# Performance work log

Hardware: AMD Instinct MI355X
Metric: run time of the kernel (lower is better)

## Reference

```python
import jax, jax.numpy as jnp
import numpy as np

N = 50000      # nodes
E = 800000     # edges (before self loops)
IN, HID, OUT = 128, 64, 64
H = 2          # heads (concat=False -> mean over heads)
NEG_SLOPE = 0.2


def setup_inputs() -> dict:
    key = jax.random.key(0)
    ks = jax.random.split(key, 10)
    s = 0.1
    x = jax.random.normal(ks[0], (N, IN), jnp.float32)
    edge_index = jax.random.randint(ks[1], (2, E), 0, N, dtype=jnp.int64)
    W1 = jax.random.normal(ks[2], (IN, H * HID), jnp.float32) * s
    att_src1 = jax.random.normal(ks[3], (H, HID), jnp.float32) * s
    att_dst1 = jax.random.normal(ks[4], (H, HID), jnp.float32) * s
    bias1 = jnp.zeros((HID,), jnp.float32)
    W2 = jax.random.normal(ks[5], (HID, H * OUT), jnp.float32) * s
    att_src2 = jax.random.normal(ks[6], (H, OUT), jnp.float32) * s
    att_dst2 = jax.random.normal(ks[7], (H, OUT), jnp.float32) * s
    bias2 = jnp.zeros((OUT,), jnp.float32)
    return dict(x=x, edge_index=edge_index, W1=W1, att_src1=att_src1,
                att_dst1=att_dst1, bias1=bias1, W2=W2, att_src2=att_src2,
                att_dst2=att_dst2, bias2=bias2)


def gat_conv(x, src, dst, W, a_src, a_dst, bias, heads, ch):
    n = x.shape[0]
    h = (x @ W).reshape(n, heads, ch)                 # [N,H,C]
    e_src = jnp.sum(h * a_src, axis=-1)               # [N,H]
    e_dst = jnp.sum(h * a_dst, axis=-1)               # [N,H]
    e = jax.nn.leaky_relu(e_src[src] + e_dst[dst], NEG_SLOPE)  # [E',H]
    # segment softmax over edges grouped by destination node
    m = jax.ops.segment_max(e, dst, num_segments=n)
    m = jnp.where(jnp.isfinite(m), m, 0.0)
    ex = jnp.exp(e - m[dst])
    denom = jax.ops.segment_sum(ex, dst, num_segments=n) + 1e-16
    alpha = ex / denom[dst]                            # [E',H]
    out = jax.ops.segment_sum(alpha[:, :, None] * h[src], dst, num_segments=n)
    return out.mean(axis=1) + bias                     # [N,C]


def reference(x, edge_index, W1, att_src1, att_dst1, bias1,
              W2, att_src2, att_dst2, bias2):
    loop = jnp.arange(N, dtype=edge_index.dtype)
    src = jnp.concatenate([edge_index[0], loop])       # add self loops
    dst = jnp.concatenate([edge_index[1], loop])
    h = gat_conv(x, src, dst, W1, att_src1, att_dst1, bias1, H, HID)
    h = jax.nn.relu(h)
    out = gat_conv(h, src, dst, W2, att_src2, att_dst2, bias2, H, OUT)
    return out
```

## Files before the change

### kernel.cpp

```cpp
#include <hip/hip_runtime.h>
#include <hip/hip_fp16.h>
#include <math.h>


#define IN_DIM 128
#define FLATC 128

__device__ __forceinline__ float lrelu02(float t) {
    return t > 0.f ? t : 0.2f * t;
}


__global__ void count_kernel(const int* __restrict__ dst, int* __restrict__ cnt, int e) {
    int i = blockIdx.x * blockDim.x + threadIdx.x;
    if (i < e) atomicAdd(&cnt[dst[i]], 1);
}

__global__ __launch_bounds__(256) void scan_bsum(const int* __restrict__ cnt,
                                                 int* __restrict__ bsum, int n) {
    __shared__ int red[256];
    int t = threadIdx.x;
    int i = blockIdx.x * 256 + t;
    red[t] = (i < n) ? cnt[i] + 1 : 0;
    __syncthreads();
#pragma unroll
    for (int off = 128; off > 0; off >>= 1) {
        if (t < off) red[t] += red[t + off];
        __syncthreads();
    }
    if (t == 0) bsum[blockIdx.x] = red[0];
}

__global__ __launch_bounds__(1024) void scan_boff(const int* __restrict__ bsum,
                                                  int* __restrict__ boff,
                                                  int* __restrict__ row_start,
                                                  int nb, int n) {
    __shared__ int s[1024];
    int t = threadIdx.x;
    int v = (t < nb) ? bsum[t] : 0;
    s[t] = v;
    __syncthreads();
    for (int off = 1; off < 1024; off <<= 1) {
        int u = (t >= off) ? s[t - off] : 0;
        __syncthreads();
        s[t] += u;
        __syncthreads();
    }
    if (t < nb) boff[t] = s[t] - v;
    if (t == nb - 1) row_start[n] = s[t];
}

__global__ __launch_bounds__(256) void scan_write(const int* __restrict__ cnt,
                                                  const int* __restrict__ boff,
                                                  int* __restrict__ row_start,
                                                  int* __restrict__ cursor,
                                                  int* __restrict__ adj, int n) {
    __shared__ int s[256];
    int t = threadIdx.x;
    int i = blockIdx.x * 256 + t;
    int v = (i < n) ? cnt[i] + 1 : 0;
    s[t] = v;
    __syncthreads();
    for (int off = 1; off < 256; off <<= 1) {
        int u = (t >= off) ? s[t - off] : 0;
        __syncthreads();
        s[t] += u;
        __syncthreads();
    }
    if (i < n) {
        int rs = boff[blockIdx.x] + s[t] - v;
        row_start[i] = rs;
        adj[rs] = i;
        cursor[i] = rs + 1;
    }
}

__global__ void scatter_kernel(const int* __restrict__ src, const int* __restrict__ dst,
                               int* __restrict__ cursor, int* __restrict__ adj, int e) {
    int i = blockIdx.x * blockDim.x + threadIdx.x;
    if (i < e) {
        int d = dst[i];
        int pos = atomicAdd(&cursor[d], 1);
        adj[pos] = src[i];
    }
}


__global__ __launch_bounds__(256) void gemm64_dots(const float* __restrict__ A,
                                                   const float* __restrict__ B,
                                                   __half* __restrict__ h16,
                                                   const float* __restrict__ att_s,
                                                   const float* __restrict__ att_d,
                                                   float2* __restrict__ es2,
                                                   float2* __restrict__ ed2,
                                                   int nrows, int K) {
    __shared__ float As[64][33];
    __shared__ float Bs[32][128];
    const int tid = threadIdx.x;
    const int tx = tid & 15;
    const int ty = tid >> 4;
    const int row0 = blockIdx.x * 64;

    float acc[4][8];
#pragma unroll
    for (int r = 0; r < 4; ++r)
#pragma unroll
        for (int c = 0; c < 8; ++c) acc[r][c] = 0.f;

    for (int k0 = 0; k0 < K; k0 += 32) {
#pragma unroll
        for (int i = 0; i < 2; ++i) {
            int idx = tid + i * 256;
            int r = idx >> 3;
            int c4 = (idx & 7) * 4;
            float4 v = make_float4(0.f, 0.f, 0.f, 0.f);
            int row = row0 + r;
            if (row < nrows) v = *(const float4*)(A + (size_t)row * K + k0 + c4);
            As[r][c4 + 0] = v.x; As[r][c4 + 1] = v.y;
            As[r][c4 + 2] = v.z; As[r][c4 + 3] = v.w;
        }
#pragma unroll
        for (int i = 0; i < 4; ++i) {
            int idx = tid + i * 256;
            int r = idx >> 5;
            int c4 = (idx & 31) * 4;
            float4 v = *(const float4*)(B + (size_t)(k0 + r) * FLATC + c4);
            *(float4*)&Bs[r][c4] = v;
        }
        __syncthreads();
#pragma unroll
        for (int kk = 0; kk < 32; ++kk) {
            float a[4], b[8];
#pragma unroll
            for (int r = 0; r < 4; ++r) a[r] = As[ty * 4 + r][kk];
#pragma unroll
            for (int c = 0; c < 8; ++c) b[c] = Bs[kk][tx + 16 * c];
#pragma unroll
            for (int r = 0; r < 4; ++r)
#pragma unroll
                for (int c = 0; c < 8; ++c) acc[r][c] = fmaf(a[r], b[c], acc[r][c]);
        }
        __syncthreads();
    }

    float asr[8], adr[8];
#pragma unroll
    for (int c = 0; c < 8; ++c) {
        asr[c] = att_s[tx + 16 * c];
        adr[c] = att_d[tx + 16 * c];
    }
#pragma unroll
    for (int r = 0; r < 4; ++r) {
        int row = row0 + ty * 4 + r;
        float s0 = 0.f, s1 = 0.f, d0 = 0.f, d1 = 0.f;
#pragma unroll
        for (int c = 0; c < 4; ++c) {
            s0 = fmaf(acc[r][c], asr[c], s0);
            d0 = fmaf(acc[r][c], adr[c], d0);
        }
#pragma unroll
        for (int c = 4; c < 8; ++c) {
            s1 = fmaf(acc[r][c], asr[c], s1);
            d1 = fmaf(acc[r][c], adr[c], d1);
        }
#pragma unroll
        for (int m = 1; m < 16; m <<= 1) {
            s0 += __shfl_xor(s0, m);
            s1 += __shfl_xor(s1, m);
            d0 += __shfl_xor(d0, m);
            d1 += __shfl_xor(d1, m);
        }
        if (row < nrows) {
#pragma unroll
            for (int c = 0; c < 8; ++c)
                h16[(size_t)row * FLATC + tx + 16 * c] = __float2half_rn(acc[r][c]);
            if (tx == 0) {
                es2[row] = make_float2(s0, s1);
                ed2[row] = make_float2(d0, d1);
            }
        }
    }
}


__global__ __launch_bounds__(256) void softmax_alpha(const int* __restrict__ row_start,
                                                     const int* __restrict__ adj,
                                                     const float2* __restrict__ es2,
                                                     const float2* __restrict__ ed2,
                                                     float2* __restrict__ alpha2,
                                                     int n) {
    int node = blockIdx.x * 4 + (threadIdx.x >> 6);
    if (node >= n) return;
    const int lane = threadIdx.x & 63;
    const int beg = row_start[node];
    const int end = row_start[node + 1];
    const float2 edv = ed2[node];

    if (end - beg <= 64) {
        int j = beg + lane;
        bool act = j < end;
        int id = adj[act ? j : beg];
        float2 ev = es2[id];
        float f0 = lrelu02(ev.x + edv.x);
        float f1 = lrelu02(ev.y + edv.y);
        float m0 = act ? f0 : -3.0e38f;
        float m1 = act ? f1 : -3.0e38f;
#pragma unroll
        for (int off = 1; off < 64; off <<= 1) {
            m0 = fmaxf(m0, __shfl_xor(m0, off));
            m1 = fmaxf(m1, __shfl_xor(m1, off));
        }
        float p0 = act ? expf(f0 - m0) : 0.f;
        float p1 = act ? expf(f1 - m1) : 0.f;
        float s0 = p0, s1 = p1;
#pragma unroll
        for (int off = 1; off < 64; off <<= 1) {
            s0 += __shfl_xor(s0, off);
            s1 += __shfl_xor(s1, off);
        }
        if (act)
            alpha2[j] = make_float2(p0 / (s0 + 1e-16f), p1 / (s1 + 1e-16f));
        return;
    }

    float m0 = -3.0e38f, m1 = -3.0e38f;
    float s0 = 0.f, s1 = 0.f;
    for (int j = beg + lane; j < end; j += 64) {
        float2 ev = es2[adj[j]];
        float f0 = lrelu02(ev.x + edv.x);
        float f1 = lrelu02(ev.y + edv.y);
        float mn0 = fmaxf(m0, f0);
        s0 = s0 * expf(m0 - mn0) + expf(f0 - mn0);
        m0 = mn0;
        float mn1 = fmaxf(m1, f1);
        s1 = s1 * expf(m1 - mn1) + expf(f1 - mn1);
        m1 = mn1;
    }
#pragma unroll
    for (int off = 1; off < 64; off <<= 1) {
        float mo0 = __shfl_xor(m0, off), so0 = __shfl_xor(s0, off);
        float mo1 = __shfl_xor(m1, off), so1 = __shfl_xor(s1, off);
        float mn0 = fmaxf(m0, mo0);
        s0 = s0 * expf(m0 - mn0) + so0 * expf(mo0 - mn0);
        m0 = mn0;
        float mn1 = fmaxf(m1, mo1);
        s1 = s1 * expf(m1 - mn1) + so1 * expf(mo1 - mn1);
        m1 = mn1;
    }
    const float inv0 = 1.f / (s0 + 1e-16f);
    const float inv1 = 1.f / (s1 + 1e-16f);
    for (int j = beg + lane; j < end; j += 64) {
        float2 ev = es2[adj[j]];
        float f0 = lrelu02(ev.x + edv.x);
        float f1 = lrelu02(ev.y + edv.y);
        alpha2[j] = make_float2(expf(f0 - m0) * inv0, expf(f1 - m1) * inv1);
    }
}


__global__ __launch_bounds__(256) void agg(const int* __restrict__ row_start,
                                           const int* __restrict__ adj,
                                           const __half2* __restrict__ h16,
                                           const float2* __restrict__ alpha2,
                                           const float* __restrict__ bias,
                                           float* __restrict__ out,
                                           int n, int do_relu) {
    int node = blockIdx.x * 4 + (threadIdx.x >> 6);
    if (node >= n) return;
    const int lane = threadIdx.x & 63;
    const int head = lane >> 5;
    const int beg = row_start[node];
    const int end = row_start[node + 1];
    const __half2* hp = h16 + lane;

    float ax = 0.f, ay = 0.f;
    int j = beg;
    for (; j + 4 <= end; j += 4) {
        int i0 = adj[j], i1 = adj[j + 1], i2 = adj[j + 2], i3 = adj[j + 3];
        float2 a0 = alpha2[j], a1 = alpha2[j + 1];
        float2 a2 = alpha2[j + 2], a3 = alpha2[j + 3];
        __half2 v0 = hp[(size_t)i0 * 64];
        __half2 v1 = hp[(size_t)i1 * 64];
        __half2 v2 = hp[(size_t)i2 * 64];
        __half2 v3 = hp[(size_t)i3 * 64];
        float w0 = head ? a0.y : a0.x;
        float w1 = head ? a1.y : a1.x;
        float w2 = head ? a2.y : a2.x;
        float w3 = head ? a3.y : a3.x;
        float2 f0 = __half22float2(v0);
        float2 f1 = __half22float2(v1);
        float2 f2 = __half22float2(v2);
        float2 f3 = __half22float2(v3);
        ax = fmaf(w0, f0.x, ax); ay = fmaf(w0, f0.y, ay);
        ax = fmaf(w1, f1.x, ax); ay = fmaf(w1, f1.y, ay);
        ax = fmaf(w2, f2.x, ax); ay = fmaf(w2, f2.y, ay);
        ax = fmaf(w3, f3.x, ax); ay = fmaf(w3, f3.y, ay);
    }
    for (; j < end; ++j) {
        int i0 = adj[j];
        float2 a0 = alpha2[j];
        float w0 = head ? a0.y : a0.x;
        float2 f0 = __half22float2(hp[(size_t)i0 * 64]);
        ax = fmaf(w0, f0.x, ax); ay = fmaf(w0, f0.y, ay);
    }

    float ox = 0.5f * (ax + __shfl_xor(ax, 32));
    float oy = 0.5f * (ay + __shfl_xor(ay, 32));
    if (lane < 32) {
        int c = 2 * lane;
        ox += bias[c];
        oy += bias[c + 1];
        if (do_relu) { ox = fmaxf(ox, 0.f); oy = fmaxf(oy, 0.f); }
        *(float2*)(out + (size_t)node * 64 + c) = make_float2(ox, oy);
    }
}


extern "C" void kernel_launch(void* const* d_in, const int* in_sizes, int n_in,
                              void* d_out, int out_size, void* d_ws, size_t ws_size,
                              hipStream_t stream) {
    const float* x   = (const float*)d_in[0];
    const int*   ei  = (const int*)d_in[1];
    const float* W1  = (const float*)d_in[2];
    const float* as1 = (const float*)d_in[3];
    const float* ad1 = (const float*)d_in[4];
    const float* b1  = (const float*)d_in[5];
    const float* W2  = (const float*)d_in[6];
    const float* as2 = (const float*)d_in[7];
    const float* ad2 = (const float*)d_in[8];
    const float* b2  = (const float*)d_in[9];

    const int N_ = in_sizes[0] / IN_DIM;
    const int E_ = in_sizes[1] / 2;
    const int* src = ei;
    const int* dst = ei + E_;
    const int TOT = E_ + N_;

    auto align16 = [](size_t v) { return (v + 15) & ~(size_t)15; };
    char* p = (char*)d_ws;
    int* cnt       = (int*)p; p += align16((size_t)N_ * 4);
    int* row_start = (int*)p; p += align16((size_t)(N_ + 1) * 4);
    int* cursor    = (int*)p; p += align16((size_t)N_ * 4);
    int* adj       = (int*)p; p += align16((size_t)TOT * 4);
    int* bsum      = (int*)p; p += align16((size_t)1024 * 4);
    int* boff      = (int*)p; p += align16((size_t)1024 * 4);
    __half* h16    = (__half*)p; p += align16((size_t)N_ * FLATC * 2);
    float* out1    = (float*)p; p += align16((size_t)N_ * 64 * 4);
    float* es      = (float*)p; p += align16((size_t)N_ * 2 * 4);
    float* ed      = (float*)p; p += align16((size_t)N_ * 2 * 4);
    float* alpha   = (float*)p; p += align16((size_t)TOT * 2 * 4);
    (void)ws_size; (void)n_in; (void)out_size;

    const int NB = (N_ + 255) / 256;

    hipMemsetAsync(cnt, 0, (size_t)N_ * 4, stream);
    count_kernel<<<(E_ + 255) / 256, 256, 0, stream>>>(dst, cnt, E_);
    scan_bsum<<<NB, 256, 0, stream>>>(cnt, bsum, N_);
    scan_boff<<<1, 1024, 0, stream>>>(bsum, boff, row_start, NB, N_);
    scan_write<<<NB, 256, 0, stream>>>(cnt, boff, row_start, cursor, adj, N_);
    scatter_kernel<<<(E_ + 255) / 256, 256, 0, stream>>>(src, dst, cursor, adj, E_);

    const int gG = (N_ + 63) / 64;
    const int gN4 = (N_ + 3) / 4;

    gemm64_dots<<<gG, 256, 0, stream>>>(x, W1, h16, as1, ad1,
                                        (float2*)es, (float2*)ed, N_, IN_DIM);
    softmax_alpha<<<gN4, 256, 0, stream>>>(row_start, adj, (const float2*)es,
                                           (const float2*)ed, (float2*)alpha, N_);
    agg<<<gN4, 256, 0, stream>>>(row_start, adj, (const __half2*)h16,
                                 (const float2*)alpha, b1, out1, N_, 1);

    gemm64_dots<<<gG, 256, 0, stream>>>(out1, W2, h16, as2, ad2,
                                        (float2*)es, (float2*)ed, N_, 64);
    softmax_alpha<<<gN4, 256, 0, stream>>>(row_start, adj, (const float2*)es,
                                           (const float2*)ed, (float2*)alpha, N_);
    agg<<<gN4, 256, 0, stream>>>(row_start, adj, (const __half2*)h16,
                                 (const float2*)alpha, b2, (float*)d_out, N_, 0);
}
```

Before: 368.3 us.

## Bucket edge scatter by destination range and vectorize GEMM shared-memory reads

The CSR build now records each edge's rank from the counting atomic. Edges are first partitioned into destination buckets of 512 nodes through per-block shared histograms, then a per-bucket kernel writes adj entries, so global writes become localized instead of randomly scattered atomics. The GEMM stores the A tile transposed and reads A and B as float4, assigning contiguous column groups per thread so fp16 outputs are written as half2. This adds an extra rank buffer, an 8-byte pair staging buffer and two more launches, and the bucket histogram assumes no more than 128 buckets.

```diff
diff --git a/kernel.cpp b/kernel.cpp
--- a/kernel.cpp
+++ b/kernel.cpp
@@ -5,15 +5,17 @@
 
 #define IN_DIM 128
 #define FLATC 128
+#define BKT_SHIFT 9
 
 __device__ __forceinline__ float lrelu02(float t) {
     return t > 0.f ? t : 0.2f * t;
 }
 
 
-__global__ void count_kernel(const int* __restrict__ dst, int* __restrict__ cnt, int e) {
+__global__ void count_kernel(const int* __restrict__ dst, int* __restrict__ cnt,
+                             int* __restrict__ rank, int e) {
     int i = blockIdx.x * blockDim.x + threadIdx.x;
-    if (i < e) atomicAdd(&cnt[dst[i]], 1);
+    if (i < e) rank[i] = atomicAdd(&cnt[dst[i]], 1);
 }
 
 __global__ __launch_bounds__(256) void scan_bsum(const int* __restrict__ cnt,
@@ -53,7 +55,6 @@
 __global__ __launch_bounds__(256) void scan_write(const int* __restrict__ cnt,
                                                   const int* __restrict__ boff,
                                                   int* __restrict__ row_start,
-                                                  int* __restrict__ cursor,
                                                   int* __restrict__ adj, int n) {
     __shared__ int s[256];
     int t = threadIdx.x;
@@ -71,17 +72,74 @@
         int rs = boff[blockIdx.x] + s[t] - v;
         row_start[i] = rs;
         adj[rs] = i;
-        cursor[i] = rs + 1;
-    }
-}
-
-__global__ void scatter_kernel(const int* __restrict__ src, const int* __restrict__ dst,
-                               int* __restrict__ cursor, int* __restrict__ adj, int e) {
-    int i = blockIdx.x * blockDim.x + threadIdx.x;
-    if (i < e) {
-        int d = dst[i];
-        int pos = atomicAdd(&cursor[d], 1);
-        adj[pos] = src[i];
+    }
+}
+
+__global__ void init_gcur(const int* __restrict__ row_start, int* __restrict__ gcur,
+                          int nbk, int n) {
+    int b = blockIdx.x * 256 + threadIdx.x;
+    if (b < nbk) {
+        int node = b << BKT_SHIFT;
+        gcur[b] = row_start[node < n ? node : n];
+    }
+}
+
+__global__ __launch_bounds__(256) void bucket_pairs(const int* __restrict__ src,
+                                                    const int* __restrict__ dst,
+                                                    const int* __restrict__ rank,
+                                                    const int* __restrict__ row_start,
+                                                    int* __restrict__ gcur,
+                                                    int2* __restrict__ bstore,
+                                                    int e, int nbk) {
+    __shared__ int hist[128], lbase[128], lcur[128];
+    const int tid = threadIdx.x;
+    const int base = blockIdx.x * 4096;
+    for (int b = tid; b < nbk; b += 256) hist[b] = 0;
+    __syncthreads();
+
+    int myb[16], mypos[16], mys[16];
+#pragma unroll
+    for (int k = 0; k < 16; ++k) {
+        int e0 = base + k * 256 + tid;
+        if (e0 < e) {
+            int d = dst[e0];
+            int b = d >> BKT_SHIFT;
+            myb[k] = b;
+            mypos[k] = row_start[d] + 1 + rank[e0];
+            mys[k] = src[e0];
+            atomicAdd(&hist[b], 1);
+        } else {
+            myb[k] = -1;
+        }
+    }
+    __syncthreads();
+    for (int b = tid; b < nbk; b += 256) {
+        int h = hist[b];
+        lbase[b] = h ? atomicAdd(&gcur[b], h) : 0;
+        lcur[b] = 0;
+    }
+    __syncthreads();
+#pragma unroll
+    for (int k = 0; k < 16; ++k) {
+        if (myb[k] >= 0) {
+            int off = atomicAdd(&lcur[myb[k]], 1);
+            bstore[lbase[myb[k]] + off] = make_int2(mypos[k], mys[k]);
+        }
+    }
+}
+
+__global__ __launch_bounds__(256) void scatter_local(const int* __restrict__ row_start,
+                                                     const int* __restrict__ gcur,
+                                                     const int2* __restrict__ bstore,
+                                                     int* __restrict__ adj,
+                                                     int n) {
+    int b = blockIdx.x;
+    int node = b << BKT_SHIFT;
+    int lo = row_start[node < n ? node : n];
+    int hi = gcur[b];
+    for (int i = lo + threadIdx.x; i < hi; i += 256) {
+        int2 p = bstore[i];
+        adj[p.x] = p.y;
     }
 }
 
@@ -94,18 +152,18 @@
                                                    float2* __restrict__ es2,
                                                    float2* __restrict__ ed2,
                                                    int nrows, int K) {
-    __shared__ float As[64][33];
+    __shared__ float Ast[32][68];
     __shared__ float Bs[32][128];
     const int tid = threadIdx.x;
     const int tx = tid & 15;
     const int ty = tid >> 4;
     const int row0 = blockIdx.x * 64;
 
-    float acc[4][8];
+    float acc0[4][4], acc1[4][4];
 #pragma unroll
     for (int r = 0; r < 4; ++r)
 #pragma unroll
-        for (int c = 0; c < 8; ++c) acc[r][c] = 0.f;
+        for (int c = 0; c < 4; ++c) { acc0[r][c] = 0.f; acc1[r][c] = 0.f; }
 
     for (int k0 = 0; k0 < K; k0 += 32) {
 #pragma unroll
@@ -116,8 +174,8 @@
             float4 v = make_float4(0.f, 0.f, 0.f, 0.f);
             int row = row0 + r;
             if (row < nrows) v = *(const float4*)(A + (size_t)row * K + k0 + c4);
-            As[r][c4 + 0] = v.x; As[r][c4 + 1] = v.y;
-            As[r][c4 + 2] = v.z; As[r][c4 + 3] = v.w;
+            Ast[c4 + 0][r] = v.x; Ast[c4 + 1][r] = v.y;
+            Ast[c4 + 2][r] = v.z; Ast[c4 + 3][r] = v.w;
         }
 #pragma unroll
         for (int i = 0; i < 4; ++i) {
@@ -130,24 +188,30 @@
         __syncthreads();
 #pragma unroll
         for (int kk = 0; kk < 32; ++kk) {
-            float a[4], b[8];
-#pragma unroll
-            for (int r = 0; r < 4; ++r) a[r] = As[ty * 4 + r][kk];
-#pragma unroll
-            for (int c = 0; c < 8; ++c) b[c] = Bs[kk][tx + 16 * c];
+            float4 a  = *(const float4*)&Ast[kk][ty * 4];
+            float4 b0 = *(const float4*)&Bs[kk][tx * 4];
+            float4 b1 = *(const float4*)&Bs[kk][64 + tx * 4];
+            const float ar[4] = {a.x, a.y, a.z, a.w};
+            const float b0r[4] = {b0.x, b0.y, b0.z, b0.w};
+            const float b1r[4] = {b1.x, b1.y, b1.z, b1.w};
 #pragma unroll
             for (int r = 0; r < 4; ++r)
 #pragma unroll
-                for (int c = 0; c < 8; ++c) acc[r][c] = fmaf(a[r], b[c], acc[r][c]);
-        }
-        __syncthreads();
-    }
-
-    float asr[8], adr[8];
-#pragma unroll
-    for (int c = 0; c < 8; ++c) {
-        asr[c] = att_s[tx + 16 * c];
-        adr[c] = att_d[tx + 16 * c];
+                for (int c = 0; c < 4; ++c) {
+                    acc0[r][c] = fmaf(ar[r], b0r[c], acc0[r][c]);
+                    acc1[r][c] = fmaf(ar[r], b1r[c], acc1[r][c]);
+                }
+        }
+        __syncthreads();
+    }
+
+    float as0[4], as1[4], ad0[4], ad1[4];
+#pragma unroll
+    for (int c = 0; c < 4; ++c) {
+        as0[c] = att_s[tx * 4 + c];
+        as1[c] = att_s[64 + tx * 4 + c];
+        ad0[c] = att_d[tx * 4 + c];
+        ad1[c] = att_d[64 + tx * 4 + c];
     }
 #pragma unroll
     for (int r = 0; r < 4; ++r) {
@@ -155,13 +219,10 @@
         float s0 = 0.f, s1 = 0.f, d0 = 0.f, d1 = 0.f;
 #pragma unroll
         for (int c = 0; c < 4; ++c) {
-            s0 = fmaf(acc[r][c], asr[c], s0);
-            d0 = fmaf(acc[r][c], adr[c], d0);
-        }
-#pragma unroll
-        for (int c = 4; c < 8; ++c) {
-            s1 = fmaf(acc[r][c], asr[c], s1);
-            d1 = fmaf(acc[r][c], adr[c], d1);
+            s0 = fmaf(acc0[r][c], as0[c], s0);
+            d0 = fmaf(acc0[r][c], ad0[c], d0);
+            s1 = fmaf(acc1[r][c], as1[c], s1);
+            d1 = fmaf(acc1[r][c], ad1[c], d1);
         }
 #pragma unroll
         for (int m = 1; m < 16; m <<= 1) {
@@ -171,9 +232,11 @@
             d1 += __shfl_xor(d1, m);
         }
         if (row < nrows) {
-#pragma unroll
-            for (int c = 0; c < 8; ++c)
-                h16[(size_t)row * FLATC + tx + 16 * c] = __float2half_rn(acc[r][c]);
+            __half* hp = h16 + (size_t)row * FLATC;
+            *(__half2*)(hp + tx * 4)      = __floats2half2_rn(acc0[r][0], acc0[r][1]);
+            *(__half2*)(hp + tx * 4 + 2)  = __floats2half2_rn(acc0[r][2], acc0[r][3]);
+            *(__half2*)(hp + 64 + tx * 4) = __floats2half2_rn(acc1[r][0], acc1[r][1]);
+            *(__half2*)(hp + 66 + tx * 4) = __floats2half2_rn(acc1[r][2], acc1[r][3]);
             if (tx == 0) {
                 es2[row] = make_float2(s0, s1);
                 ed2[row] = make_float2(d0, d1);
@@ -335,15 +398,18 @@
     const int* src = ei;
     const int* dst = ei + E_;
     const int TOT = E_ + N_;
+    const int NBK = (N_ + (1 << BKT_SHIFT) - 1) >> BKT_SHIFT;
 
     auto align16 = [](size_t v) { return (v + 15) & ~(size_t)15; };
     char* p = (char*)d_ws;
     int* cnt       = (int*)p; p += align16((size_t)N_ * 4);
     int* row_start = (int*)p; p += align16((size_t)(N_ + 1) * 4);
-    int* cursor    = (int*)p; p += align16((size_t)N_ * 4);
+    int* rank      = (int*)p; p += align16((size_t)E_ * 4);
     int* adj       = (int*)p; p += align16((size_t)TOT * 4);
     int* bsum      = (int*)p; p += align16((size_t)1024 * 4);
     int* boff      = (int*)p; p += align16((size_t)1024 * 4);
+    int* gcur      = (int*)p; p += align16((size_t)128 * 4);
+    int2* bstore   = (int2*)p; p += align16((size_t)TOT * 8);
     __half* h16    = (__half*)p; p += align16((size_t)N_ * FLATC * 2);
     float* out1    = (float*)p; p += align16((size_t)N_ * 64 * 4);
     float* es      = (float*)p; p += align16((size_t)N_ * 2 * 4);
@@ -354,11 +420,14 @@
     const int NB = (N_ + 255) / 256;
 
     hipMemsetAsync(cnt, 0, (size_t)N_ * 4, stream);
-    count_kernel<<<(E_ + 255) / 256, 256, 0, stream>>>(dst, cnt, E_);
+    count_kernel<<<(E_ + 255) / 256, 256, 0, stream>>>(dst, cnt, rank, E_);
     scan_bsum<<<NB, 256, 0, stream>>>(cnt, bsum, N_);
     scan_boff<<<1, 1024, 0, stream>>>(bsum, boff, row_start, NB, N_);
-    scan_write<<<NB, 256, 0, stream>>>(cnt, boff, row_start, cursor, adj, N_);
-    scatter_kernel<<<(E_ + 255) / 256, 256, 0, stream>>>(src, dst, cursor, adj, E_);
+    scan_write<<<NB, 256, 0, stream>>>(cnt, boff, row_start, adj, N_);
+    init_gcur<<<1, 256, 0, stream>>>(row_start, gcur, NBK, N_);
+    bucket_pairs<<<(E_ + 4095) / 4096, 256, 0, stream>>>(src, dst, rank, row_start,
+                                                         gcur, bstore, E_, NBK);
+    scatter_local<<<NBK, 256, 0, stream>>>(row_start, gcur, bstore, adj, N_);
 
     const int gG = (N_ + 63) / 64;
     const int gN4 = (N_ + 3) / 4;
```

Result: faster. 338.7 us (-8.0%).
